# Kernel optimization log

Measured on AMD Instinct MI355X. Metric: run time of the kernel, lower is better.

The kernel has to match this reference:

```python
import jax, jax.numpy as jnp
import numpy as np
import math

# ---- static config (matches init_kwargs) ----
MUL = 16                       # multiplicity of 0e and 1o irreps in/out
IN_DIM = 4 * MUL               # 16x0e + 16x1o -> 16 + 48 = 64 channels
DIAMETER = 7.0
RADIUS = DIAMETER / 2.0
NRB = 8                        # num_radial_basis
STEPS = (1.0, 1.0, 1.0)
N_PATHS = 5                    # 0x0->0, 1x1->0, 0x1->1, 1x0->1, 1x1->1
WEIGHT_NUMEL = N_PATHS * MUL * MUL  # 1280


def _lattice():
    axes = []
    for st in STEPS:
        s = math.floor(RADIUS / st)
        axes.append(np.arange(-s, s + 1.0) * st)
    return np.stack(np.meshgrid(*axes, indexing='ij'), axis=-1).astype(np.float32)  # [kx,ky,kz,3]


def _radial_emb(r):
    # e3nn soft_one_hot_linspace, basis='smooth_finite', cutoff=True
    values = np.linspace(0.0, RADIUS, NRB + 2)[1:-1].astype(np.float32)
    step = values[1] - values[0]
    diff = (r[..., None] - values) / step
    def u(t):  # soft unit step: exp(-1/t) for t>0 else 0
        return np.where(t > 0.0, np.exp(-1.0 / np.where(t > 0.0, t, 1.0)), 0.0)
    return (1.14136 * math.e ** 2 * u(diff + 1.0) * u(1.0 - diff)).astype(np.float32)


def _spherical_harmonics(lat):
    # normalize=True, normalization='component': Y0 = 1, Y1 = sqrt(3) * unit_vec
    n = np.linalg.norm(lat, axis=-1, keepdims=True)
    unit = np.where(n > 0, lat / np.where(n > 0, n, 1.0), 0.0)
    return np.ones(lat.shape[:-1], np.float32), (math.sqrt(3.0) * unit).astype(np.float32)


_LAT = _lattice()
_EMB = jnp.asarray(_radial_emb(np.linalg.norm(_LAT, axis=-1)))  # [kx,ky,kz,NRB]
_sh0_np, _sh1_np = _spherical_harmonics(_LAT)
_SH0, _SH1 = jnp.asarray(_sh0_np), jnp.asarray(_sh1_np)
_eps_np = np.zeros((3, 3, 3), np.float32)
for _i, _j, _k in [(0, 1, 2), (1, 2, 0), (2, 0, 1)]:
    _eps_np[_i, _j, _k] = 1.0
    _eps_np[_i, _k, _j] = -1.0
_EPS = jnp.asarray(_eps_np)


def _build_kernel(tp_weight):
    """Radial-basis matmul + CG tensor-product -> conv kernel [out,in,kx,ky,kz]."""
    kx, ky, kz = _LAT.shape[:3]
    nk = kx * ky * kz
    w = jnp.einsum('xyzb,bn->xyzn', _EMB, tp_weight) / nk
    w = w.reshape(kx, ky, kz, N_PATHS, MUL, MUL)
    w1, w2, w3, w4, w5 = [w[..., p, :, :] for p in range(N_PATHS)]
    # e3nn path weights ('component' norm, 'element' path norm): sqrt(dim_out / fan_in)
    a0 = math.sqrt(1.0 / (2 * MUL))  # -> 0e: paths 1,2 each mul1*mul2 = MUL
    a1 = math.sqrt(3.0 / (3 * MUL))  # -> 1o: paths 3,4,5
    c1 = a0                          # w3j(0,0,0) = 1
    c2 = a0 / math.sqrt(3.0)         # w3j(1,1,0) = delta/sqrt(3)
    c3 = a1 / math.sqrt(3.0)         # w3j(0,1,1) = delta/sqrt(3)
    c4 = a1 / math.sqrt(3.0)         # w3j(1,0,1) = delta/sqrt(3)
    c5 = a1 / math.sqrt(6.0)         # w3j(1,1,1) = eps/sqrt(6)
    Kss = c1 * _SH0[..., None, None] * w1                                  # [k,u,o]
    Kvs = c2 * jnp.einsum('xyzi,xyzuo->xyzuio', _SH1, w2)                  # [k,u,3,o]
    Ksv = c3 * jnp.einsum('xyzk,xyzuo->xyzuok', _SH1, w3)                  # [k,u,o,3]
    eye3 = jnp.eye(3, dtype=w.dtype)
    Kvv = (c4 * jnp.einsum('xyz,ik,xyzuo->xyzuiok', _SH0, eye3, w4)
           + c5 * jnp.einsum('ijk,xyzj,xyzuo->xyzuiok', _EPS, _SH1, w5))   # [k,u,3,o,3]
    top = jnp.concatenate([Kss, Ksv.reshape(kx, ky, kz, MUL, 3 * MUL)], axis=-1)
    bot = jnp.concatenate([Kvs.reshape(kx, ky, kz, 3 * MUL, MUL),
                           Kvv.reshape(kx, ky, kz, 3 * MUL, 3 * MUL)], axis=-1)
    K = jnp.concatenate([top, bot], axis=-2)                               # [kx,ky,kz,in,out]
    return jnp.transpose(K, (4, 3, 0, 1, 2))                               # oixyz


def setup_inputs() -> dict:
    key = jax.random.key(0)
    k1, k2, k3, k4 = jax.random.split(key, 4)
    x = jax.random.normal(k1, (2, IN_DIM, 40, 40, 40), jnp.float32)
    sc_w0 = jax.random.normal(k2, (MUL, MUL), jnp.float32)
    sc_w1 = jax.random.normal(k3, (MUL, MUL), jnp.float32)
    tp_weight = jax.random.normal(k4, (NRB, WEIGHT_NUMEL), jnp.float32)
    return {"x": x, "sc_w0": sc_w0, "sc_w1": sc_w1, "tp_weight": tp_weight}


def reference(x, sc_w0, sc_w1, tp_weight):
    B = x.shape[0]
    sp = x.shape[2:]
    inv = 1.0 / math.sqrt(MUL)  # e3nn Linear fan-in normalization
    x0 = x[:, :MUL]                                  # [B,MUL,D,H,W]
    x1 = x[:, MUL:].reshape(B, MUL, 3, *sp)          # [B,MUL,3,D,H,W]
    sc0 = jnp.einsum('uo,budhw->bodhw', sc_w0, x0) * inv
    sc1 = jnp.einsum('uo,buidhw->boidhw', sc_w1, x1) * inv
    sc = jnp.concatenate([sc0, sc1.reshape(B, 3 * MUL, *sp)], axis=1)
    K = _build_kernel(tp_weight)
    pad = [(s // 2, s // 2) for s in K.shape[2:]]
    conv = jax.lax.conv_general_dilated(
        x, K, window_strides=(1, 1, 1), padding=pad,
        dimension_numbers=('NCDHW', 'OIDHW', 'NCDHW'))
    return sc + conv
```

## Files before the change

### kernel.cpp

```cpp
#include <hip/hip_runtime.h>
#include <stdint.h>


#define NT_REAL 179
#define NT_PAD  180
#define NPAIR   90

#define XCH  1557376
#define XCHB ((size_t)XCH * 2)

#define HBYTES 50176
#define SEGB   12288
#define NSEG   15
#define NSTEP  120

typedef short s16x8 __attribute__((ext_vector_type(8)));
typedef float f32x4 __attribute__((ext_vector_type(4)));
typedef float f32x16 __attribute__((ext_vector_type(16)));

struct Taps {
  int n;
  short dl16[NT_PAD];
  unsigned char dz[NT_PAD], dy[NT_PAD], dx[NT_PAD];
};
constexpr Taps mk_taps() {
  Taps t{};
  t.n = 0;
  for (int a = 0; a < 7; ++a)
    for (int b = 0; b < 7; ++b)
      for (int c = 0; c < 7; ++c) {
        int d2 = (a-3)*(a-3) + (b-3)*(b-3) + (c-3)*(c-3);
        if (d2 <= 12) {
          t.dz[t.n] = (unsigned char)a; t.dy[t.n] = (unsigned char)b;
          t.dx[t.n] = (unsigned char)c;
          t.dl16[t.n] = (short)((a*14 + b)*16 + c);
          ++t.n;
        }
      }
  for (int i = t.n; i < NT_PAD; ++i) {
    t.dz[i] = 3; t.dy[i] = 3; t.dx[i] = 3; t.dl16[i] = t.dl16[0];
  }
  return t;
}
__device__ constexpr Taps TAPS = mk_taps();
static_assert(mk_taps().n == NT_REAL, "tap count");

struct DL2 { unsigned int v[NPAIR]; };
constexpr DL2 mk_dl2() {
  DL2 d{};
  Taps t = mk_taps();
  for (int p = 0; p < NPAIR; ++p)
    d.v[p] = (unsigned int)(unsigned short)t.dl16[2*p]
           | ((unsigned int)(unsigned short)t.dl16[2*p + 1] << 16);
  return d;
}
__device__ constexpr DL2 DL2V = mk_dl2();

static __device__ inline unsigned short f2bf(float f) {
  unsigned int u = __float_as_uint(f);
  unsigned int r = u + 0x7FFFu + ((u >> 16) & 1u);
  return (unsigned short)(r >> 16);
}

__device__ __forceinline__ void gl_lds16(const void* g, void* s) {
  __builtin_amdgcn_global_load_lds(
      (const __attribute__((address_space(1))) void*)g,
      (__attribute__((address_space(3))) void*)s, 16, 0, 0);
}

__global__ void prep(const float* __restrict__ x, const float* __restrict__ scw0,
                     const float* __restrict__ scw1, const float* __restrict__ tpw,
                     unsigned short* __restrict__ Xp, unsigned short* __restrict__ Bwp) {
  __shared__ float buf[160 * 65];
  int tid = threadIdx.x;

  if (blockIdx.x < 800) {
    int blk = blockIdx.x;
    int ys = blk % 10; int t2 = blk / 10; int iz = t2 % 40; int b = t2 / 40;
    int y0 = ys * 4;
    const float* src = x + (size_t)b * 4096000 + (size_t)iz * 1600 + (size_t)y0 * 40;
    for (int e = tid; e < 64 * 160; e += 256) {
      int ch = e / 160, i = e - ch * 160;
      buf[i * 65 + ch] = src[(size_t)ch * 64000 + i];
    }
    __syncthreads();
    for (int f = tid; f < 160 * 8; f += 256) {
      int i = f >> 3, g = f & 7;
      int yy = i / 40, xx = i - yy * 40;
      s16x8 v;
      #pragma unroll
      for (int j = 0; j < 8; ++j) v[j] = (short)f2bf(buf[i * 65 + g * 8 + j]);
      size_t pos = ((size_t)((b * 46 + iz + 3) * 46 + (y0 + yy + 3)) * 46 + (xx + 3));
      *reinterpret_cast<s16x8*>(Xp + (size_t)g * XCH + pos * 8) = v;
    }
    return;
  }

  int t = blockIdx.x - 800;
  float (*wsm)[16][16] = reinterpret_cast<float (*)[16][16]>(buf);

  int dz = TAPS.dz[t], dy = TAPS.dy[t], dx = TAPS.dx[t];
  float fz = dz - 3.0f, fy = dy - 3.0f, fx = dx - 3.0f;
  float d2 = fz*fz + fy*fy + fx*fx;
  float r = sqrtf(d2);

  const float step = 3.5f / 9.0f;
  const float Cc = 1.14136f * 7.38905609893065f;
  float emb[8];
  for (int bb = 0; bb < 8; ++bb) {
    float diff = (r - step * (bb + 1)) / step;
    float t1 = diff + 1.0f, t2 = 1.0f - diff;
    float u1 = (t1 > 0.0f) ? expf(-1.0f / t1) : 0.0f;
    float u2 = (t2 > 0.0f) ? expf(-1.0f / t2) : 0.0f;
    emb[bb] = Cc * u1 * u2;
  }

  int u = tid >> 4, o = tid & 15;
  for (int p = 0; p < 5; ++p) {
    float acc = 0.0f;
    int nidx = (p * 16 + u) * 16 + o;
    for (int bb = 0; bb < 8; ++bb) acc += emb[bb] * tpw[bb * 1280 + nidx];
    wsm[p][u][o] = acc * (1.0f / 343.0f);
  }
  __syncthreads();

  float invr = (d2 > 0.0f) ? (1.7320508075688772f / r) : 0.0f;
  float sh[3] = { fz * invr, fy * invr, fx * invr };

  bool center = (dz == 3 && dy == 3 && dx == 3);
  bool padt = (t >= NT_REAL);
  const float c1 = 0.17677669529663687f;
  const float c2 = 0.10206207261596575f;
  const float c3 = 0.14433756729740643f;
  const float c4 = 0.14433756729740643f;
  const float c5 = 0.10206207261596575f;
  const float inv = 0.25f;

  for (int e = tid; e < 4096; e += 256) {
    int ich = e & 63, och = e >> 6;
    float v = 0.0f;
    if (!padt) {
      if (och < 16) {
        if (ich < 16) {
          v = c1 * wsm[0][ich][och];
          if (center) v += inv * scw0[ich * 16 + och];
        } else {
          int qq = ich - 16; int uu = qq / 3, ii = qq % 3;
          v = c2 * sh[ii] * wsm[1][uu][och];
        }
      } else {
        int qo = och - 16; int oo = qo / 3, kk = qo % 3;
        if (ich < 16) {
          v = c3 * sh[kk] * wsm[2][ich][oo];
        } else {
          int qi = ich - 16; int uu = qi / 3, ii = qi % 3;
          if (ii == kk) {
            v = c4 * wsm[3][uu][oo];
            if (center) v += inv * scw1[uu * 16 + oo];
          } else {
            int jj = 3 - ii - kk;
            float sgn = (((kk - ii + 3) % 3) == 2) ? 1.0f : -1.0f;
            v = c5 * sgn * sh[jj] * wsm[4][uu][oo];
          }
        }
      }
    }
    int chunk = ich >> 3, j = ich & 7;
    int pair = t >> 1, hi = t & 1;
    int og = och >> 5, col = och & 31;
    size_t idx = ((((size_t)chunk * NPAIR + pair) * 2 + og) * 2 + hi) * 256
               + (size_t)col * 8 + j;
    Bwp[idx] = f2bf(v);
  }
}

__global__ __launch_bounds__(256, 1) void conv3d(
    const unsigned short* __restrict__ Xp,
    const unsigned short* __restrict__ Bwp,
    float* __restrict__ out) {
  __shared__ __align__(16) unsigned char smem[2 * HBYTES + 4 * SEGB];
  unsigned char* BB = smem + 2 * HBYTES;

  int blk = blockIdx.x;
  int p = ((blk & 7) << 5) | (blk >> 3);
  if (p >= 250) return;
  int b = p / 125; int rem = p - b * 125;
  int tz = rem / 25, ty = (rem / 5) % 5, tx = rem % 5;

  int tid = threadIdx.x;
  int lane = tid & 63;
  int w = tid >> 6;
  int hi = lane >> 5, r32 = lane & 31;
  int hs = hi << 4;

  size_t hbase = (size_t)(((b * 46 + tz * 8) * 46 + ty * 8) * 46 + tx * 8) * 16;

  int abase = w * 448 + ((r32 >> 3) << 4) + (r32 & 7);

  f32x16 acc[4][2];
  #pragma unroll
  for (int f = 0; f < 4; ++f)
    #pragma unroll
    for (int og = 0; og < 2; ++og)
      #pragma unroll
      for (int e = 0; e < 16; ++e) acc[f][og][e] = 0.0f;

  auto stageB = [&](int st) {
    int cn = st / NSEG, sn = st - cn * NSEG;
    const unsigned char* bg = (const unsigned char*)Bwp
        + ((size_t)cn * NPAIR + sn * 6) * 2048;
    unsigned char* dst = BB + (size_t)(st & 3) * SEGB;
    for (int k = w; k < 12; k += 4)
      gl_lds16(bg + (k << 10) + lane * 16, dst + (k << 10));
  };
  auto stageHLine = [&](int c, int k, unsigned char* dst) {
    const unsigned char* xc = (const unsigned char*)Xp + (size_t)c * XCHB + hbase;
    int sl = (k << 6) + lane;
    int hx = sl & 15; hx = hx > 13 ? 13 : hx;
    int r = sl >> 4;
    int hz = (r * 2341) >> 15;
    int hy = r - hz * 14;
    gl_lds16(xc + ((size_t)((hz * 46 + hy) * 46 + hx)) * 16, dst + (k << 10));
  };

  for (int k = w; k < 49; k += 4) stageHLine(0, k, smem);
  stageB(0); stageB(1); stageB(2);
  asm volatile("s_waitcnt vmcnt(6)" ::: "memory");
  __builtin_amdgcn_s_barrier();

  int t = 0;
  for (int c = 0; c < 8; ++c) {
    unsigned char* XH  = smem + (c & 1) * HBYTES;
    unsigned char* XHn = smem + ((c + 1) & 1) * HBYTES;
    for (int s = 0; s < NSEG; ++s, ++t) {
      if (t + 3 < NSTEP) stageB(t + 3);
      if (c + 1 < 8) {
        int L = s * 4 + w;
        if (L < 49) stageHLine(c + 1, L, XHn);
      }

      const unsigned char* BSc = BB + (size_t)(t & 3) * SEGB + (size_t)lane * 16;
      s16x8 fa[2][4], fb[2][2];
      {
        unsigned int dlv = DL2V.v[s * 6];
        int dl = (int)((dlv >> hs) & 0xFFFFu);
        const unsigned char* ab = XH + ((size_t)(abase + dl) << 4);
        fa[0][0] = *(const s16x8*)(ab);
        fa[0][1] = *(const s16x8*)(ab + 1024);
        fa[0][2] = *(const s16x8*)(ab + 3584);
        fa[0][3] = *(const s16x8*)(ab + 4608);
        fb[0][0] = *(const s16x8*)(BSc);
        fb[0][1] = *(const s16x8*)(BSc + 1024);
      }
      #pragma unroll
      for (int pp = 0; pp < 6; ++pp) {
        int cur = pp & 1, nxt = cur ^ 1;
        if (pp < 5) {
          unsigned int dlv = DL2V.v[s * 6 + pp + 1];
          int dl = (int)((dlv >> hs) & 0xFFFFu);
          const unsigned char* ab = XH + ((size_t)(abase + dl) << 4);
          fa[nxt][0] = *(const s16x8*)(ab);
          fa[nxt][1] = *(const s16x8*)(ab + 1024);
          fa[nxt][2] = *(const s16x8*)(ab + 3584);
          fa[nxt][3] = *(const s16x8*)(ab + 4608);
          const unsigned char* bp = BSc + ((pp + 1) << 11);
          fb[nxt][0] = *(const s16x8*)(bp);
          fb[nxt][1] = *(const s16x8*)(bp + 1024);
        }
        acc[0][0] = __builtin_amdgcn_mfma_f32_32x32x16_bf16(fa[cur][0], fb[cur][0], acc[0][0], 0, 0, 0);
        acc[0][1] = __builtin_amdgcn_mfma_f32_32x32x16_bf16(fa[cur][0], fb[cur][1], acc[0][1], 0, 0, 0);
        acc[1][0] = __builtin_amdgcn_mfma_f32_32x32x16_bf16(fa[cur][1], fb[cur][0], acc[1][0], 0, 0, 0);
        acc[1][1] = __builtin_amdgcn_mfma_f32_32x32x16_bf16(fa[cur][1], fb[cur][1], acc[1][1], 0, 0, 0);
        acc[2][0] = __builtin_amdgcn_mfma_f32_32x32x16_bf16(fa[cur][2], fb[cur][0], acc[2][0], 0, 0, 0);
        acc[2][1] = __builtin_amdgcn_mfma_f32_32x32x16_bf16(fa[cur][2], fb[cur][1], acc[2][1], 0, 0, 0);
        acc[3][0] = __builtin_amdgcn_mfma_f32_32x32x16_bf16(fa[cur][3], fb[cur][0], acc[3][0], 0, 0, 0);
        acc[3][1] = __builtin_amdgcn_mfma_f32_32x32x16_bf16(fa[cur][3], fb[cur][1], acc[3][1], 0, 0, 0);
      }

      if (t <= NSTEP - 4)      asm volatile("s_waitcnt vmcnt(6)" ::: "memory");
      else if (t == NSTEP - 3) asm volatile("s_waitcnt vmcnt(3)" ::: "memory");
      else                     asm volatile("s_waitcnt vmcnt(0)" ::: "memory");
      __builtin_amdgcn_s_barrier();
    }
  }

  int col = lane & 31;
  #pragma unroll
  for (int og = 0; og < 2; ++og) {
    #pragma unroll
    for (int f = 0; f < 4; ++f) {
      int zz = f >> 1, aq = f & 1;
      size_t cb = (size_t)(b * 64 + og * 32 + col) * 64000
                + (size_t)(tz * 8 + 2 * w + zz) * 1600
                + (size_t)(tx * 8 + hi * 4);
      #pragma unroll
      for (int ys = 0; ys < 4; ++ys) {
        float* dst = out + cb + (size_t)(ty * 8 + aq * 4 + ys) * 40;
        f32x4 v = { acc[f][og][ys * 4 + 0], acc[f][og][ys * 4 + 1],
                    acc[f][og][ys * 4 + 2], acc[f][og][ys * 4 + 3] };
        *reinterpret_cast<f32x4*>(dst) = v;
      }
    }
  }
}

extern "C" void kernel_launch(void* const* d_in, const int* in_sizes, int n_in,
                              void* d_out, int out_size, void* d_ws, size_t ws_size,
                              hipStream_t stream) {
  const float* x    = (const float*)d_in[0];
  const float* scw0 = (const float*)d_in[1];
  const float* scw1 = (const float*)d_in[2];
  const float* tpw  = (const float*)d_in[3];
  float* out = (float*)d_out;

  unsigned short* Xp  = (unsigned short*)d_ws;
  unsigned short* Bwp = Xp + (size_t)8 * XCH;

  hipMemsetAsync(Xp, 0, (size_t)8 * XCH * 2, stream);
  prep<<<800 + NT_PAD, 256, 0, stream>>>(x, scw0, scw1, tpw, Xp, Bwp);
  conv3d<<<256, 256, 0, stream>>>(Xp, Bwp, out);
}
```

Measured before the change: 264.4 us.

## Halve conv3d z-tile and run two blocks per CU with single-buffered halo

Shrinks each block's output tile from 8 to 4 z-planes, which doubles the grid to 500 active blocks. Launch bounds become two blocks per CU. The halo tile in LDS is now single-buffered and loaded with a barrier at each channel-chunk boundary. The weight-segment ring drops from 4 to 3 slots so LDS fits two resident blocks, and s_setprio is raised around the MFMA loop. The intent is to use all CUs and let the co-resident block hide halo-load stalls. The cost is more halo traffic per output and more B-fragment LDS reads per MFMA.

```diff
diff --git a/kernel.cpp b/kernel.cpp
--- a/kernel.cpp
+++ b/kernel.cpp
@@ -9,7 +9,7 @@
 #define XCH  1557376
 #define XCHB ((size_t)XCH * 2)
 
-#define HBYTES 50176
+#define HBYTES 35840
 #define SEGB   12288
 #define NSEG   15
 #define NSTEP  120
@@ -174,17 +174,17 @@
   }
 }
 
-__global__ __launch_bounds__(256, 1) void conv3d(
+__global__ __launch_bounds__(256, 2) void conv3d(
     const unsigned short* __restrict__ Xp,
     const unsigned short* __restrict__ Bwp,
     float* __restrict__ out) {
-  __shared__ __align__(16) unsigned char smem[2 * HBYTES + 4 * SEGB];
-  unsigned char* BB = smem + 2 * HBYTES;
+  __shared__ __align__(16) unsigned char smem[HBYTES + 3 * SEGB];
+  unsigned char* BB = smem + HBYTES;
 
   int blk = blockIdx.x;
-  int p = ((blk & 7) << 5) | (blk >> 3);
-  if (p >= 250) return;
-  int b = p / 125; int rem = p - b * 125;
+  int p = ((blk & 7) << 6) | (blk >> 3);
+  if (p >= 500) return;
+  int b = p / 250; int rem = p - b * 250;
   int tz = rem / 25, ty = (rem / 5) % 5, tx = rem % 5;
 
   int tid = threadIdx.x;
@@ -193,13 +193,13 @@
   int hi = lane >> 5, r32 = lane & 31;
   int hs = hi << 4;
 
-  size_t hbase = (size_t)(((b * 46 + tz * 8) * 46 + ty * 8) * 46 + tx * 8) * 16;
-
-  int abase = w * 448 + ((r32 >> 3) << 4) + (r32 & 7);
-
-  f32x16 acc[4][2];
+  size_t hbase = (size_t)(((b * 46 + tz * 4) * 46 + ty * 8) * 46 + tx * 8) * 16;
+
+  int abase = w * 224 + ((r32 >> 3) << 4) + (r32 & 7);
+
+  f32x16 acc[2][2];
   #pragma unroll
-  for (int f = 0; f < 4; ++f)
+  for (int f = 0; f < 2; ++f)
     #pragma unroll
     for (int og = 0; og < 2; ++og)
       #pragma unroll
@@ -209,60 +209,59 @@
     int cn = st / NSEG, sn = st - cn * NSEG;
     const unsigned char* bg = (const unsigned char*)Bwp
         + ((size_t)cn * NPAIR + sn * 6) * 2048;
-    unsigned char* dst = BB + (size_t)(st & 3) * SEGB;
+    unsigned char* dst = BB + (size_t)(st % 3) * SEGB;
     for (int k = w; k < 12; k += 4)
       gl_lds16(bg + (k << 10) + lane * 16, dst + (k << 10));
   };
-  auto stageHLine = [&](int c, int k, unsigned char* dst) {
+  auto stageH = [&](int c) {
     const unsigned char* xc = (const unsigned char*)Xp + (size_t)c * XCHB + hbase;
-    int sl = (k << 6) + lane;
-    int hx = sl & 15; hx = hx > 13 ? 13 : hx;
-    int r = sl >> 4;
-    int hz = (r * 2341) >> 15;
-    int hy = r - hz * 14;
-    gl_lds16(xc + ((size_t)((hz * 46 + hy) * 46 + hx)) * 16, dst + (k << 10));
+    for (int k = w; k < 35; k += 4) {
+      int sl = (k << 6) + lane;
+      int hx = sl & 15; hx = hx > 13 ? 13 : hx;
+      int r = sl >> 4;
+      int hz = (r * 2341) >> 15;
+      int hy = r - hz * 14;
+      gl_lds16(xc + ((size_t)((hz * 46 + hy) * 46 + hx)) * 16, smem + (k << 10));
+    }
   };
 
-  for (int k = w; k < 49; k += 4) stageHLine(0, k, smem);
-  stageB(0); stageB(1); stageB(2);
-  asm volatile("s_waitcnt vmcnt(6)" ::: "memory");
+  stageH(0);
+  stageB(0); stageB(1);
+  asm volatile("s_waitcnt vmcnt(3)" ::: "memory");
   __builtin_amdgcn_s_barrier();
 
   int t = 0;
   for (int c = 0; c < 8; ++c) {
-    unsigned char* XH  = smem + (c & 1) * HBYTES;
-    unsigned char* XHn = smem + ((c + 1) & 1) * HBYTES;
+    if (c > 0) {
+      stageH(c);
+      stageB(t + 1);
+      asm volatile("s_waitcnt vmcnt(3)" ::: "memory");
+      __builtin_amdgcn_s_barrier();
+    }
     for (int s = 0; s < NSEG; ++s, ++t) {
-      if (t + 3 < NSTEP) stageB(t + 3);
-      if (c + 1 < 8) {
-        int L = s * 4 + w;
-        if (L < 49) stageHLine(c + 1, L, XHn);
-      }
-
-      const unsigned char* BSc = BB + (size_t)(t & 3) * SEGB + (size_t)lane * 16;
-      s16x8 fa[2][4], fb[2][2];
+      if (s < 14 && t + 2 < NSTEP) stageB(t + 2);
+
+      const unsigned char* BSc = BB + (size_t)(t % 3) * SEGB + (size_t)lane * 16;
+      s16x8 fa[2][2], fb[2][2];
       {
         unsigned int dlv = DL2V.v[s * 6];
         int dl = (int)((dlv >> hs) & 0xFFFFu);
-        const unsigned char* ab = XH + ((size_t)(abase + dl) << 4);
+        const unsigned char* ab = smem + ((size_t)(abase + dl) << 4);
         fa[0][0] = *(const s16x8*)(ab);
         fa[0][1] = *(const s16x8*)(ab + 1024);
-        fa[0][2] = *(const s16x8*)(ab + 3584);
-        fa[0][3] = *(const s16x8*)(ab + 4608);
         fb[0][0] = *(const s16x8*)(BSc);
         fb[0][1] = *(const s16x8*)(BSc + 1024);
       }
+      __builtin_amdgcn_s_setprio(1);
       #pragma unroll
       for (int pp = 0; pp < 6; ++pp) {
         int cur = pp & 1, nxt = cur ^ 1;
         if (pp < 5) {
           unsigned int dlv = DL2V.v[s * 6 + pp + 1];
           int dl = (int)((dlv >> hs) & 0xFFFFu);
-          const unsigned char* ab = XH + ((size_t)(abase + dl) << 4);
+          const unsigned char* ab = smem + ((size_t)(abase + dl) << 4);
           fa[nxt][0] = *(const s16x8*)(ab);
           fa[nxt][1] = *(const s16x8*)(ab + 1024);
-          fa[nxt][2] = *(const s16x8*)(ab + 3584);
-          fa[nxt][3] = *(const s16x8*)(ab + 4608);
           const unsigned char* bp = BSc + ((pp + 1) << 11);
           fb[nxt][0] = *(const s16x8*)(bp);
           fb[nxt][1] = *(const s16x8*)(bp + 1024);
@@ -271,15 +270,13 @@
         acc[0][1] = __builtin_amdgcn_mfma_f32_32x32x16_bf16(fa[cur][0], fb[cur][1], acc[0][1], 0, 0, 0);
         acc[1][0] = __builtin_amdgcn_mfma_f32_32x32x16_bf16(fa[cur][1], fb[cur][0], acc[1][0], 0, 0, 0);
         acc[1][1] = __builtin_amdgcn_mfma_f32_32x32x16_bf16(fa[cur][1], fb[cur][1], acc[1][1], 0, 0, 0);
-        acc[2][0] = __builtin_amdgcn_mfma_f32_32x32x16_bf16(fa[cur][2], fb[cur][0], acc[2][0], 0, 0, 0);
-        acc[2][1] = __builtin_amdgcn_mfma_f32_32x32x16_bf16(fa[cur][2], fb[cur][1], acc[2][1], 0, 0, 0);
-        acc[3][0] = __builtin_amdgcn_mfma_f32_32x32x16_bf16(fa[cur][3], fb[cur][0], acc[3][0], 0, 0, 0);
-        acc[3][1] = __builtin_amdgcn_mfma_f32_32x32x16_bf16(fa[cur][3], fb[cur][1], acc[3][1], 0, 0, 0);
-      }
-
-      if (t <= NSTEP - 4)      asm volatile("s_waitcnt vmcnt(6)" ::: "memory");
-      else if (t == NSTEP - 3) asm volatile("s_waitcnt vmcnt(3)" ::: "memory");
-      else                     asm volatile("s_waitcnt vmcnt(0)" ::: "memory");
+      }
+      __builtin_amdgcn_s_setprio(0);
+
+      if (s < 14 && t < NSTEP - 2)
+        asm volatile("s_waitcnt vmcnt(3)" ::: "memory");
+      else
+        asm volatile("s_waitcnt vmcnt(0)" ::: "memory");
       __builtin_amdgcn_s_barrier();
     }
   }
@@ -288,14 +285,13 @@
   #pragma unroll
   for (int og = 0; og < 2; ++og) {
     #pragma unroll
-    for (int f = 0; f < 4; ++f) {
-      int zz = f >> 1, aq = f & 1;
+    for (int f = 0; f < 2; ++f) {
       size_t cb = (size_t)(b * 64 + og * 32 + col) * 64000
-                + (size_t)(tz * 8 + 2 * w + zz) * 1600
+                + (size_t)(tz * 4 + w) * 1600
                 + (size_t)(tx * 8 + hi * 4);
       #pragma unroll
       for (int ys = 0; ys < 4; ++ys) {
-        float* dst = out + cb + (size_t)(ty * 8 + aq * 4 + ys) * 40;
+        float* dst = out + cb + (size_t)(ty * 8 + f * 4 + ys) * 40;
         f32x4 v = { acc[f][og][ys * 4 + 0], acc[f][og][ys * 4 + 1],
                     acc[f][og][ys * 4 + 2], acc[f][og][ys * 4 + 3] };
         *reinterpret_cast<f32x4*>(dst) = v;
@@ -318,5 +314,5 @@
 
   hipMemsetAsync(Xp, 0, (size_t)8 * XCH * 2, stream);
   prep<<<800 + NT_PAD, 256, 0, stream>>>(x, scw0, scw1, tpw, Xp, Bwp);
-  conv3d<<<256, 256, 0, stream>>>(Xp, Bwp, out);
-}
+  conv3d<<<512, 256, 0, stream>>>(Xp, Bwp, out);
+}
```

After: 261.9 us. Within noise of the previous version (-1.0%).
